# Optimization experiments

Measured on AMD Instinct MI355X. Metric: run time of the kernel, lower is better.

Reference implementation:

```python
import jax, jax.numpy as jnp
import numpy as np

SPATIAL_SHAPES = ((128, 128), (64, 64), (32, 32), (16, 16))  # (h, w) per level
N_HEADS, N_LEVELS, N_POINTS, D_MODEL = 8, 4, 4, 256


def setup_inputs() -> dict:
    key = jax.random.key(0)
    ks = jax.random.split(key, 10)
    bs, nq, nk = 4, 300, 17
    inp = {
        'query': jax.random.normal(ks[0], (bs, nq * nk, D_MODEL), jnp.float32),
        'reference_points': jax.random.uniform(ks[1], (bs, nq, N_LEVELS, nk, 2), jnp.float32),
    }
    for l, (h, w) in enumerate(SPATIAL_SHAPES):
        inp[f'value{l}'] = jax.random.normal(ks[2 + l], (bs * N_HEADS, D_MODEL // N_HEADS, h * w), jnp.float32)
    inp['W_off'] = jax.random.normal(ks[6], (N_HEADS * N_LEVELS * N_POINTS * 2, D_MODEL), jnp.float32) * 0.02
    inp['b_off'] = jax.random.normal(ks[7], (N_HEADS * N_LEVELS * N_POINTS * 2,), jnp.float32) * 0.5
    inp['W_attn'] = jax.random.normal(ks[8], (N_HEADS * N_LEVELS * N_POINTS, D_MODEL), jnp.float32) * 0.02
    inp['b_attn'] = jax.random.normal(ks[9], (N_HEADS * N_LEVELS * N_POINTS,), jnp.float32) * 0.02
    return inp


def _bilinear_sample(v, grid, h, w):
    # v: (N, C, h*w); grid: (N, P, 2) normalized to [-1, 1] (x, y).
    # F.grid_sample bilinear, padding_mode='zeros', align_corners=False.
    x = (grid[..., 0] + 1.0) * 0.5 * w - 0.5
    y = (grid[..., 1] + 1.0) * 0.5 * h - 0.5
    x0 = jnp.floor(x)
    y0 = jnp.floor(y)
    wx1, wy1 = x - x0, y - y0
    wx0, wy0 = 1.0 - wx1, 1.0 - wy1
    x0i, y0i = x0.astype(jnp.int32), y0.astype(jnp.int32)
    out = 0.0
    for xi, yi, wgt in ((x0i, y0i, wx0 * wy0), (x0i + 1, y0i, wx1 * wy0),
                        (x0i, y0i + 1, wx0 * wy1), (x0i + 1, y0i + 1, wx1 * wy1)):
        valid = (xi >= 0) & (xi < w) & (yi >= 0) & (yi < h)
        idx = jnp.clip(yi, 0, h - 1) * w + jnp.clip(xi, 0, w - 1)       # (N, P)
        g = jnp.take_along_axis(v, idx[:, None, :], axis=2)              # (N, C, P)
        out = out + g * (wgt * valid.astype(v.dtype))[:, None, :]
    return out


def reference(query, reference_points, value0, value1, value2, value3, W_off, b_off, W_attn, b_attn):
    bs, len_q, _ = query.shape
    hd = D_MODEL // N_HEADS
    values = (value0, value1, value2, value3)

    off = (query @ W_off.T + b_off).reshape(bs, len_q, N_HEADS, N_LEVELS, N_POINTS, 2)
    attn = (query @ W_attn.T + b_attn).reshape(bs, len_q, N_HEADS, N_LEVELS * N_POINTS)
    attn = jax.nn.softmax(attn, axis=-1)

    # (bs, nq, L, nk, 2) -> transpose(2,3) -> flatten(1,2) -> (bs, len_q, L, 2)
    rp = jnp.transpose(reference_points, (0, 1, 3, 2, 4)).reshape(bs, len_q, N_LEVELS, 2)
    # normalizer: spatial (h, w) flipped -> (w, h)
    norm = jnp.array([[w, h] for (h, w) in SPATIAL_SHAPES], dtype=query.dtype).reshape(1, 1, 1, N_LEVELS, 1, 2)
    loc = rp[:, :, None, :, None, :] + off / norm                         # (bs, len_q, H, L, P, 2)

    grids = 2.0 * loc - 1.0
    grids = jnp.transpose(grids, (0, 2, 1, 3, 4, 5)).reshape(bs * N_HEADS, len_q, N_LEVELS, N_POINTS, 2)

    sampled = []
    for l, (h, w) in enumerate(SPATIAL_SHAPES):
        g = grids[:, :, l].reshape(bs * N_HEADS, len_q * N_POINTS, 2)
        s = _bilinear_sample(values[l], g, h, w)                          # (bs*H, hd, len_q*P)
        sampled.append(s.reshape(bs * N_HEADS, hd, len_q, N_POINTS))
    sampled = jnp.concatenate(sampled, axis=-1)                           # (bs*H, hd, len_q, L*P)

    attn_r = jnp.transpose(attn, (0, 2, 1, 3)).reshape(bs * N_HEADS, 1, len_q, N_LEVELS * N_POINTS)
    out = (sampled * attn_r).sum(-1).reshape(bs, D_MODEL, len_q)
    return jnp.transpose(out, (0, 2, 1))                                  # (bs, len_q, d_model)
```

## Files before the change

kernel.cpp:

```cpp
#include <hip/hip_runtime.h>
#include <math.h>

#define BS        4
#define NQ        300
#define NK        17
#define LEN_Q     5100
#define N_HEADS   8
#define N_LEVELS  4
#define N_POINTS  4
#define D_MODEL   256
#define HD        32

#define LB0 0
#define LB1 16777216
#define LB2 20971520
#define LB3 22020096
#define VT_TOTAL 22282240

typedef __attribute__((ext_vector_type(8))) short bf16x8;
typedef __attribute__((ext_vector_type(8))) unsigned short ushort8_t;
typedef __attribute__((ext_vector_type(4))) float f32x4;

__device__ __forceinline__ unsigned short f2bf(float x) {
    unsigned u = __float_as_uint(x);
    unsigned r = (u + 0x7fffu + ((u >> 16) & 1u)) >> 16;
    return (unsigned short)r;
}
__device__ __forceinline__ float bf2f(unsigned short s) {
    return __uint_as_float((unsigned)s << 16);
}
__device__ __forceinline__ bf16x8 cvt8(const float* __restrict__ p) {
    float4 a = *(const float4*)p;
    float4 b = *(const float4*)(p + 4);
    bf16x8 r;
    r[0] = f2bf(a.x); r[1] = f2bf(a.y); r[2] = f2bf(a.z); r[3] = f2bf(a.w);
    r[4] = f2bf(b.x); r[5] = f2bf(b.y); r[6] = f2bf(b.z); r[7] = f2bf(b.w);
    return r;
}

__global__ __launch_bounds__(256) void transpose_bf16_kernel(
    const float* __restrict__ v0, const float* __restrict__ v1,
    const float* __restrict__ v2, const float* __restrict__ v3,
    unsigned short* __restrict__ vt)
{
    __shared__ float t[32][36];
    int bx = blockIdx.x;
    int n  = blockIdx.y;

    const float* in; int S; size_t ob; int tile;
    if (bx < 512)      { in = v0; S = 16384; ob = LB0; tile = bx; }
    else if (bx < 640) { in = v1; S = 4096;  ob = LB1; tile = bx - 512; }
    else if (bx < 672) { in = v2; S = 1024;  ob = LB2; tile = bx - 640; }
    else               { in = v3; S = 256;   ob = LB3; tile = bx - 672; }

    int tid = threadIdx.x;
    int s0 = tile * 32;

    int c  = tid >> 3;
    int c4 = (tid & 7) * 4;
    const float* pin = in + (size_t)n * 32 * S;
    *(float4*)&t[c][c4] = *(const float4*)(pin + (size_t)c * S + s0 + c4);
    __syncthreads();

    unsigned short* pout = vt + ob + (size_t)n * S * 32;
    int r = tid >> 3;
    ushort4 w;
    w.x = f2bf(t[c4 + 0][r]);
    w.y = f2bf(t[c4 + 1][r]);
    w.z = f2bf(t[c4 + 2][r]);
    w.w = f2bf(t[c4 + 3][r]);
    *(ushort4*)(pout + (size_t)(s0 + r) * 32 + c4) = w;
}

__global__ __launch_bounds__(256) void proj_gemm_mfma(
    const float* __restrict__ Q,
    const float* __restrict__ Woff, const float* __restrict__ boff,
    const float* __restrict__ Wattn, const float* __restrict__ battn,
    float* __restrict__ P, int M)
{
    int tid  = threadIdx.x;
    int wave = tid >> 6;
    int lane = tid & 63;
    int bm = blockIdx.y * 64;
    int bn = blockIdx.x * 128;
    int wm = (wave & 1) * 32;
    int wn = (wave >> 1) * 64;
    int lr = lane & 15;
    int lk = (lane >> 4) * 8;

    f32x4 acc[2][4] = {};
    for (int k0 = 0; k0 < 256; k0 += 32) {
        bf16x8 afrag[2], bfrag[4];
        #pragma unroll
        for (int i = 0; i < 2; ++i) {
            int row = bm + wm + i * 16 + lr;
            row = row < M ? row : M - 1;
            afrag[i] = cvt8(Q + (size_t)row * 256 + k0 + lk);
        }
        #pragma unroll
        for (int j = 0; j < 4; ++j) {
            int n = bn + wn + j * 16 + lr;
            const float* wp = (n < 256) ? (Woff + (size_t)n * 256)
                                        : (Wattn + (size_t)(n - 256) * 256);
            bfrag[j] = cvt8(wp + k0 + lk);
        }
        #pragma unroll
        for (int i = 0; i < 2; ++i)
            #pragma unroll
            for (int j = 0; j < 4; ++j)
                acc[i][j] = __builtin_amdgcn_mfma_f32_16x16x32_bf16(
                    afrag[i], bfrag[j], acc[i][j], 0, 0, 0);
    }

    #pragma unroll
    for (int i = 0; i < 2; ++i) {
        int mbase = bm + wm + i * 16 + (lane >> 4) * 4;
        #pragma unroll
        for (int j = 0; j < 4; ++j) {
            int n = bn + wn + j * 16 + (lane & 15);
            float bias = (n < 256) ? boff[n] : battn[n - 256];
            #pragma unroll
            for (int r = 0; r < 4; ++r) {
                int row = mbase + r;
                if (row < M) P[(size_t)row * 384 + n] = acc[i][j][r] + bias;
            }
        }
    }
}

#define ACCUM(Ax, Bx, U0, U1, U2, U3)                                          \
  { float w0 = __int_as_float(Ax.y), w1 = __int_as_float(Ax.w);                \
    float w2 = __int_as_float(Bx.y), w3 = __int_as_float(Bx.w);                \
    accA.x += w0*bf2f(U0[0]) + w1*bf2f(U1[0]) + w2*bf2f(U2[0]) + w3*bf2f(U3[0]); \
    accA.y += w0*bf2f(U0[1]) + w1*bf2f(U1[1]) + w2*bf2f(U2[1]) + w3*bf2f(U3[1]); \
    accA.z += w0*bf2f(U0[2]) + w1*bf2f(U1[2]) + w2*bf2f(U2[2]) + w3*bf2f(U3[2]); \
    accA.w += w0*bf2f(U0[3]) + w1*bf2f(U1[3]) + w2*bf2f(U2[3]) + w3*bf2f(U3[3]); \
    accB.x += w0*bf2f(U0[4]) + w1*bf2f(U1[4]) + w2*bf2f(U2[4]) + w3*bf2f(U3[4]); \
    accB.y += w0*bf2f(U0[5]) + w1*bf2f(U1[5]) + w2*bf2f(U2[5]) + w3*bf2f(U3[5]); \
    accB.z += w0*bf2f(U0[6]) + w1*bf2f(U1[6]) + w2*bf2f(U2[6]) + w3*bf2f(U3[6]); \
    accB.w += w0*bf2f(U0[7]) + w1*bf2f(U1[7]) + w2*bf2f(U2[7]) + w3*bf2f(U3[7]); }

#define RED(v) { v += __shfl_xor(v, 4); v += __shfl_xor(v, 8); }

__global__ __launch_bounds__(256) void ms_deform_kernel(
    const float* __restrict__ rp,
    const float* __restrict__ proj,
    const unsigned short* __restrict__ vt,
    float* __restrict__ out)
{
    int bid = blockIdx.x;
    int h   = bid & 7;
    int b   = (bid >> 3) & 3;
    int qc  = bid >> 5;
    int q0  = qc * 16;

    __shared__ int s_iw[3104];

    int tid = threadIdx.x;

    {
        int qL = tid >> 4;
        int lp = tid & 15;
        int l  = lp >> 2;
        int p  = lp & 3;
        int q  = q0 + qL;
        int qq = q < LEN_Q ? q : LEN_Q - 1;
        const float* prow = proj + (size_t)(b * LEN_Q + qq) * 384;

        float g = prow[256 + h * 16 + lp];
        float mx = g;
        mx = fmaxf(mx, __shfl_xor(mx, 1, 16));
        mx = fmaxf(mx, __shfl_xor(mx, 2, 16));
        mx = fmaxf(mx, __shfl_xor(mx, 4, 16));
        mx = fmaxf(mx, __shfl_xor(mx, 8, 16));
        float e = __expf(g - mx);
        float s = e;
        s += __shfl_xor(s, 1, 16);
        s += __shfl_xor(s, 2, 16);
        s += __shfl_xor(s, 4, 16);
        s += __shfl_xor(s, 8, 16);
        float a = (q < LEN_Q) ? (e / s) : 0.f;

        int Wl = 128 >> l;
        float ww = (float)Wl;
        int qi = qq / NK;
        int ki = qq - qi * NK;
        size_t rbase = ((((size_t)b * NQ + qi) * N_LEVELS + l) * NK + ki) * 2;
        float rx = rp[rbase + 0];
        float ry = rp[rbase + 1];
        int oj = (h * 16 + lp) * 2;
        float ox = prow[oj], oy = prow[oj + 1];
        float x = (rx + ox / ww) * ww - 0.5f;
        float y = (ry + oy / ww) * ww - 0.5f;
        float x0f = floorf(x), y0f = floorf(y);
        float wx1 = x - x0f, wy1 = y - y0f;
        float wx0 = 1.f - wx1, wy0 = 1.f - wy1;
        int x0 = (int)x0f, y0 = (int)y0f;

        int* wrow = s_iw + (qL >> 1) * 388 + (p * 8 + l * 2 + (qL & 1)) * 12;
        #pragma unroll
        for (int corner = 0; corner < 4; ++corner) {
            int xi = x0 + (corner & 1);
            int yi = y0 + (corner >> 1);
            float wgt = ((corner & 1) ? wx1 : wx0) * ((corner >> 1) ? wy1 : wy0);
            bool valid = (xi >= 0) && (xi < Wl) && (yi >= 0) && (yi < Wl);
            int2 iw;
            iw.x = valid ? (yi * Wl + xi) * HD : 0;
            iw.y = __float_as_int(valid ? wgt * a : 0.f);
            *(int2*)(wrow + corner * 2) = iw;
        }
    }
    __syncthreads();

    int qL = tid >> 4;
    int l  = (tid >> 2) & 3;
    int c8 = tid & 3;
    int n  = b * N_HEADS + h;
    const size_t lb[4]  = {LB0, LB1, LB2, LB3};
    const int    Ssz[4] = {16384, 4096, 1024, 256};

    const unsigned short* vbase = vt + lb[l] + (size_t)n * Ssz[l] * HD + c8 * 8;
    const int* rrow0 = s_iw + (qL >> 1) * 388 + (l * 2 + (qL & 1)) * 12;

    int4 A0 = *(const int4*)(rrow0 + 0);
    int4 B0 = *(const int4*)(rrow0 + 4);
    int4 A1 = *(const int4*)(rrow0 + 96);
    int4 B1 = *(const int4*)(rrow0 + 100);
    int4 A2 = *(const int4*)(rrow0 + 192);
    int4 B2 = *(const int4*)(rrow0 + 196);
    int4 A3 = *(const int4*)(rrow0 + 288);
    int4 B3 = *(const int4*)(rrow0 + 292);

    ushort8_t u00 = *(const ushort8_t*)(vbase + A0.x);
    ushort8_t u01 = *(const ushort8_t*)(vbase + A0.z);
    ushort8_t u02 = *(const ushort8_t*)(vbase + B0.x);
    ushort8_t u03 = *(const ushort8_t*)(vbase + B0.z);
    ushort8_t u10 = *(const ushort8_t*)(vbase + A1.x);
    ushort8_t u11 = *(const ushort8_t*)(vbase + A1.z);
    ushort8_t u12 = *(const ushort8_t*)(vbase + B1.x);
    ushort8_t u13 = *(const ushort8_t*)(vbase + B1.z);
    ushort8_t u20 = *(const ushort8_t*)(vbase + A2.x);
    ushort8_t u21 = *(const ushort8_t*)(vbase + A2.z);
    ushort8_t u22 = *(const ushort8_t*)(vbase + B2.x);
    ushort8_t u23 = *(const ushort8_t*)(vbase + B2.z);
    ushort8_t u30 = *(const ushort8_t*)(vbase + A3.x);
    ushort8_t u31 = *(const ushort8_t*)(vbase + A3.z);
    ushort8_t u32 = *(const ushort8_t*)(vbase + B3.x);
    ushort8_t u33 = *(const ushort8_t*)(vbase + B3.z);

    float4 accA = make_float4(0.f, 0.f, 0.f, 0.f);
    float4 accB = make_float4(0.f, 0.f, 0.f, 0.f);
    ACCUM(A0, B0, u00, u01, u02, u03)
    ACCUM(A1, B1, u10, u11, u12, u13)
    ACCUM(A2, B2, u20, u21, u22, u23)
    ACCUM(A3, B3, u30, u31, u32, u33)

    RED(accA.x) RED(accA.y) RED(accA.z) RED(accA.w)
    RED(accB.x) RED(accB.y) RED(accB.z) RED(accB.w)

    if ((tid & 12) == 0) {
        int q = q0 + qL;
        if (q < LEN_Q) {
            float* po = out + (size_t)(b * LEN_Q + q) * 256 + h * 32 + c8 * 8;
            *(float4*)po = accA;
            *(float4*)(po + 4) = accB;
        }
    }
}

extern "C" void kernel_launch(void* const* d_in, const int* in_sizes, int n_in,
                              void* d_out, int out_size, void* d_ws, size_t ws_size,
                              hipStream_t stream)
{
    const float* query = (const float*)d_in[0];
    const float* refp  = (const float*)d_in[1];
    const float* v0    = (const float*)d_in[2];
    const float* v1    = (const float*)d_in[3];
    const float* v2    = (const float*)d_in[4];
    const float* v3    = (const float*)d_in[5];
    const float* Woff  = (const float*)d_in[6];
    const float* boff  = (const float*)d_in[7];
    const float* Wattn = (const float*)d_in[8];
    const float* battn = (const float*)d_in[9];
    float* out = (float*)d_out;
    unsigned short* vt = (unsigned short*)d_ws;
    float* proj = (float*)(vt + VT_TOTAL);

    int M = BS * LEN_Q;

    transpose_bf16_kernel<<<dim3(680, 32), 256, 0, stream>>>(
        v0, v1, v2, v3, vt);

    proj_gemm_mfma<<<dim3(3, (M + 63) / 64), 256, 0, stream>>>(
        query, Woff, boff, Wattn, battn, proj, M);

    ms_deform_kernel<<<319 * 32, 256, 0, stream>>>(refp, proj, vt, out);
}
```

Measured before the change: 117.3 us.

## Pre-convert query and weights to bf16 before projection GEMM, shrink N tile

Adds a separate kernel that converts the query and both weight matrices to bf16 once in workspace, so the projection GEMM loads bf16 fragments directly instead of loading fp32 and converting inline. The GEMM N tile is halved to 64 with twice as many blocks along N, which raises parallelism and lowers per-wave accumulator registers. In exchange there is an extra launch and an extra read and write pass over the query.

```diff
diff --git a/kernel.cpp b/kernel.cpp
--- a/kernel.cpp
+++ b/kernel.cpp
@@ -16,6 +16,8 @@
 #define LB2 20971520
 #define LB3 22020096
 #define VT_TOTAL 22282240
+#define PROJ_F32 7833600
+#define QB_N     5222400
 
 typedef __attribute__((ext_vector_type(8))) short bf16x8;
 typedef __attribute__((ext_vector_type(8))) unsigned short ushort8_t;
@@ -29,13 +31,31 @@
 __device__ __forceinline__ float bf2f(unsigned short s) {
     return __uint_as_float((unsigned)s << 16);
 }
-__device__ __forceinline__ bf16x8 cvt8(const float* __restrict__ p) {
-    float4 a = *(const float4*)p;
-    float4 b = *(const float4*)(p + 4);
-    bf16x8 r;
+
+__global__ __launch_bounds__(256) void cvt_bf16_kernel(
+    const float* __restrict__ Q, const float* __restrict__ Woff,
+    const float* __restrict__ Wattn,
+    unsigned short* __restrict__ Qb, unsigned short* __restrict__ Wb)
+{
+    int gid = blockIdx.x * 256 + threadIdx.x;
+    const float* src;
+    unsigned short* dst;
+    size_t off;
+    if (gid < 652800) {
+        src = Q; dst = Qb; off = (size_t)gid * 8;
+    } else {
+        int wg = gid - 652800;
+        off = (size_t)wg * 8;
+        dst = Wb;
+        if (off < 65536) { src = Woff; }
+        else             { src = Wattn; src -= 65536; }
+    }
+    float4 a = *(const float4*)(src + off);
+    float4 b = *(const float4*)(src + off + 4);
+    ushort8_t r;
     r[0] = f2bf(a.x); r[1] = f2bf(a.y); r[2] = f2bf(a.z); r[3] = f2bf(a.w);
     r[4] = f2bf(b.x); r[5] = f2bf(b.y); r[6] = f2bf(b.z); r[7] = f2bf(b.w);
-    return r;
+    *(ushort8_t*)(dst + off) = r;
 }
 
 __global__ __launch_bounds__(256) void transpose_bf16_kernel(
@@ -73,50 +93,46 @@
 }
 
 __global__ __launch_bounds__(256) void proj_gemm_mfma(
-    const float* __restrict__ Q,
-    const float* __restrict__ Woff, const float* __restrict__ boff,
-    const float* __restrict__ Wattn, const float* __restrict__ battn,
+    const unsigned short* __restrict__ Qb,
+    const unsigned short* __restrict__ Wb,
+    const float* __restrict__ boff, const float* __restrict__ battn,
     float* __restrict__ P, int M)
 {
     int tid  = threadIdx.x;
     int wave = tid >> 6;
     int lane = tid & 63;
     int bm = blockIdx.y * 64;
-    int bn = blockIdx.x * 128;
+    int bn = blockIdx.x * 64;
     int wm = (wave & 1) * 32;
-    int wn = (wave >> 1) * 64;
+    int wn = (wave >> 1) * 32;
     int lr = lane & 15;
     int lk = (lane >> 4) * 8;
 
-    f32x4 acc[2][4] = {};
+    int ra0 = bm + wm + lr;       ra0 = ra0 < M ? ra0 : M - 1;
+    int ra1 = bm + wm + 16 + lr;  ra1 = ra1 < M ? ra1 : M - 1;
+    const unsigned short* qa0 = Qb + (size_t)ra0 * 256 + lk;
+    const unsigned short* qa1 = Qb + (size_t)ra1 * 256 + lk;
+    const unsigned short* wb0 = Wb + (size_t)(bn + wn + lr) * 256 + lk;
+    const unsigned short* wb1 = Wb + (size_t)(bn + wn + 16 + lr) * 256 + lk;
+
+    f32x4 acc[2][2] = {};
+    #pragma unroll
     for (int k0 = 0; k0 < 256; k0 += 32) {
-        bf16x8 afrag[2], bfrag[4];
-        #pragma unroll
-        for (int i = 0; i < 2; ++i) {
-            int row = bm + wm + i * 16 + lr;
-            row = row < M ? row : M - 1;
-            afrag[i] = cvt8(Q + (size_t)row * 256 + k0 + lk);
-        }
-        #pragma unroll
-        for (int j = 0; j < 4; ++j) {
-            int n = bn + wn + j * 16 + lr;
-            const float* wp = (n < 256) ? (Woff + (size_t)n * 256)
-                                        : (Wattn + (size_t)(n - 256) * 256);
-            bfrag[j] = cvt8(wp + k0 + lk);
-        }
-        #pragma unroll
-        for (int i = 0; i < 2; ++i)
-            #pragma unroll
-            for (int j = 0; j < 4; ++j)
-                acc[i][j] = __builtin_amdgcn_mfma_f32_16x16x32_bf16(
-                    afrag[i], bfrag[j], acc[i][j], 0, 0, 0);
+        bf16x8 a0 = *(const bf16x8*)(qa0 + k0);
+        bf16x8 a1 = *(const bf16x8*)(qa1 + k0);
+        bf16x8 b0 = *(const bf16x8*)(wb0 + k0);
+        bf16x8 b1 = *(const bf16x8*)(wb1 + k0);
+        acc[0][0] = __builtin_amdgcn_mfma_f32_16x16x32_bf16(a0, b0, acc[0][0], 0, 0, 0);
+        acc[0][1] = __builtin_amdgcn_mfma_f32_16x16x32_bf16(a0, b1, acc[0][1], 0, 0, 0);
+        acc[1][0] = __builtin_amdgcn_mfma_f32_16x16x32_bf16(a1, b0, acc[1][0], 0, 0, 0);
+        acc[1][1] = __builtin_amdgcn_mfma_f32_16x16x32_bf16(a1, b1, acc[1][1], 0, 0, 0);
     }
 
     #pragma unroll
     for (int i = 0; i < 2; ++i) {
         int mbase = bm + wm + i * 16 + (lane >> 4) * 4;
         #pragma unroll
-        for (int j = 0; j < 4; ++j) {
+        for (int j = 0; j < 2; ++j) {
             int n = bn + wn + j * 16 + (lane & 15);
             float bias = (n < 256) ? boff[n] : battn[n - 256];
             #pragma unroll
@@ -285,14 +301,18 @@
     float* out = (float*)d_out;
     unsigned short* vt = (unsigned short*)d_ws;
     float* proj = (float*)(vt + VT_TOTAL);
+    unsigned short* Qb = (unsigned short*)(proj + PROJ_F32);
+    unsigned short* Wb = Qb + QB_N;
 
     int M = BS * LEN_Q;
 
     transpose_bf16_kernel<<<dim3(680, 32), 256, 0, stream>>>(
         v0, v1, v2, v3, vt);
 
-    proj_gemm_mfma<<<dim3(3, (M + 63) / 64), 256, 0, stream>>>(
-        query, Woff, boff, Wattn, battn, proj, M);
+    cvt_bf16_kernel<<<2598, 256, 0, stream>>>(query, Woff, Wattn, Qb, Wb);
+
+    proj_gemm_mfma<<<dim3(6, (M + 63) / 64), 256, 0, stream>>>(
+        Qb, Wb, boff, battn, proj, M);
 
     ms_deform_kernel<<<319 * 32, 256, 0, stream>>>(refp, proj, vt, out);
 }
```

Result: faster. 110.5 us (-5.8%).
